# Kernel tuning notes

Hardware: AMD Instinct MI355X
Metric: run time of the kernel (lower is better)

## Reference

```python
import jax, jax.numpy as jnp
import numpy as np
from jax import lax

S, L, V, E, H, FA, HOP, NL = 512, 128, 50000, 256, 256, 128, 4, 16


def setup_inputs() -> dict:
    key = jax.random.key(0)
    ks = jax.random.split(key, 25)
    def rn(k, shape, s=0.05):
        return jax.random.normal(k, shape, dtype=jnp.float32) * s
    inp = {}
    inp['tokens'] = jax.random.randint(ks[0], (S, L), 0, V)
    inp['emb'] = rn(ks[1], (V, E), 0.1)
    # token bi-LSTM, pytorch gate layout (i,f,g,o) stacked in dim 0
    inp['tWih_f'] = rn(ks[2], (4*H, E)); inp['tWhh_f'] = rn(ks[3], (4*H, H))
    inp['tbih_f'] = rn(ks[4], (4*H,));  inp['tbhh_f'] = rn(ks[5], (4*H,))
    inp['tWih_b'] = rn(ks[6], (4*H, E)); inp['tWhh_b'] = rn(ks[7], (4*H, H))
    inp['tbih_b'] = rn(ks[8], (4*H,));  inp['tbhh_b'] = rn(ks[9], (4*H,))
    inp['attW'] = rn(ks[10], (FA, H)); inp['attb'] = rn(ks[11], (FA,))
    inp['ctx'] = rn(ks[12], (HOP, FA))
    D2 = H * HOP
    inp['sWih_f'] = rn(ks[13], (4*HOP, D2)); inp['sWhh_f'] = rn(ks[14], (4*HOP, HOP))
    inp['sbih_f'] = rn(ks[15], (4*HOP,));    inp['sbhh_f'] = rn(ks[16], (4*HOP,))
    inp['sWih_b'] = rn(ks[17], (4*HOP, D2)); inp['sWhh_b'] = rn(ks[18], (4*HOP, HOP))
    inp['sbih_b'] = rn(ks[19], (4*HOP,));    inp['sbhh_b'] = rn(ks[20], (4*HOP,))
    inp['linW'] = rn(ks[21], (NL, HOP), 0.3); inp['linb'] = rn(ks[22], (NL,), 0.3)
    inp['trans'] = rn(ks[23], (NL, NL), 1.0)
    return inp


def _lstm_dir(x, Wih, Whh, bih, bhh, reverse):
    # x: [B, T, D] -> [B, T, Hh]
    if reverse:
        x = x[:, ::-1]
    B = x.shape[0]
    Hh = Whh.shape[1]
    def step(carry, xt):
        h, c = carry
        g = xt @ Wih.T + bih + h @ Whh.T + bhh
        i, f, gg, o = jnp.split(g, 4, axis=-1)
        c = jax.nn.sigmoid(f) * c + jax.nn.sigmoid(i) * jnp.tanh(gg)
        h = jax.nn.sigmoid(o) * jnp.tanh(c)
        return (h, c), h
    h0 = jnp.zeros((B, Hh), x.dtype)
    _, hs = lax.scan(step, (h0, h0), x.transpose(1, 0, 2))
    out = hs.transpose(1, 0, 2)
    return out[:, ::-1] if reverse else out


def _bilstm_sum(x, Wf, Uf, bif, bhf, Wb, Ub, bib, bhb):
    # bidirectional LSTM; module sums fwd/bwd halves of concat output
    return (_lstm_dir(x, Wf, Uf, bif, bhf, False)
            + _lstm_dir(x, Wb, Ub, bib, bhb, True))


def _viterbi(p, T):
    # max-plus recurrence: v_n[j] = p_n[j] + max_i(v_{n-1}[i] + T[i,j])
    def step(v, pn):
        v2 = pn + jnp.max(v[:, None] + T, axis=0)
        return v2, v2
    v0 = p[0]
    _, vs = lax.scan(step, v0, p[1:])
    return jnp.concatenate([v0[None, :], vs], axis=0)  # [S, NL]


def reference(tokens, emb, tWih_f, tWhh_f, tbih_f, tbhh_f, tWih_b, tWhh_b,
              tbih_b, tbhh_b, attW, attb, ctx, sWih_f, sWhh_f, sbih_f, sbhh_f,
              sWih_b, sWhh_b, sbih_b, sbhh_b, linW, linb, trans):
    x = emb[tokens]                                   # [S, L, E] gather
    enc = _bilstm_sum(x, tWih_f, tWhh_f, tbih_f, tbhh_f,
                      tWih_b, tWhh_b, tbih_b, tbhh_b)  # [S, L, H]
    hidden = enc @ attW.T + attb                       # [S, L, FA]
    scores = hidden @ ctx.T                            # [S, L, HOP]
    attn = jax.nn.softmax(scores, axis=1)              # softmax over token axis
    sent = jnp.einsum('sld,slh->sdh', enc, attn)       # [S, H, HOP]
    sent = sent.reshape(1, sent.shape[0], -1)          # [1, S, H*HOP]
    senc = _bilstm_sum(sent, sWih_f, sWhh_f, sbih_f, sbhh_f,
                       sWib := sWih_b, sWhh_b, sbih_b, sbhh_b)  # [1, S, HOP]
    pf = senc @ linW.T + linb                          # [1, S, NL]
    return _viterbi(pf[0], trans)                      # [S, NL]
```

## Files before the change

### kernel.cpp

```cpp
#include <hip/hip_runtime.h>
#include <hip/hip_bf16.h>

typedef __attribute__((ext_vector_type(8))) short short8;
typedef __attribute__((ext_vector_type(4))) float f32x4;

__device__ __forceinline__ float b2f(unsigned short u) {
    union { unsigned int i; float f; } v; v.i = ((unsigned int)u) << 16; return v.f;
}
__device__ __forceinline__ unsigned short f2b(float f) {
    union { float f; unsigned int i; } v; v.f = f;
    return (unsigned short)((v.i + 0x7FFFu + ((v.i >> 16) & 1u)) >> 16);
}
__device__ __forceinline__ float sig_f(float x) {
    return __builtin_amdgcn_rcpf(1.f + __expf(-x));
}
__device__ __forceinline__ float tanh_f(float x) {
    return 1.f - 2.f * __builtin_amdgcn_rcpf(1.f + __expf(2.f * x));
}
__device__ __forceinline__ void gll16(const void* g, void* lds) {
    __builtin_amdgcn_global_load_lds(
        (const __attribute__((address_space(1))) unsigned int*)g,
        (__attribute__((address_space(3))) unsigned int*)lds, 16, 0, 0);
}

__global__ void k_prep(const float* __restrict__ Wih_f, const float* __restrict__ Whh_f,
                       const float* __restrict__ bih_f, const float* __restrict__ bhh_f,
                       const float* __restrict__ Wih_b, const float* __restrict__ Whh_b,
                       const float* __restrict__ bih_b, const float* __restrict__ bhh_b,
                       const float* __restrict__ attW,
                       short* __restrict__ Wfrag, float* __restrict__ biasp,
                       short* __restrict__ attWfrag)
{
    int idx = blockIdx.x * blockDim.x + threadIdx.x;
    if (idx < 2 * 1024 * 512) {
        int j = idx & 7, lane = (idx >> 3) & 63, b = idx >> 9;
        int gt = b & 3, kk = (b >> 2) & 15, ng = (b >> 6) & 15, dir = b >> 10;
        int u = lane & 15;
        int k = kk * 32 + (lane >> 4) * 8 + j;
        int row = gt * 256 + ng * 16 + u;
        const float* Wih = dir ? Wih_b : Wih_f;
        const float* Whh = dir ? Whh_b : Whh_f;
        float val = (k < 256) ? Wih[row * 256 + k] : Whh[row * 256 + (k - 256)];
        Wfrag[idx] = (short)f2b(val);
    } else if (idx < 2 * 1024 * 512 + 2048) {
        int i = idx - 2 * 1024 * 512;
        int dir = i >> 10, col = i & 1023;
        int ng = col >> 6, rem = col & 63, gt = rem >> 4, u = rem & 15;
        int row = gt * 256 + ng * 16 + u;
        biasp[i] = dir ? (bih_b[row] + bhh_b[row]) : (bih_f[row] + bhh_f[row]);
    } else if (idx < 2 * 1024 * 512 + 2048 + 32768) {
        int o = idx - (2 * 1024 * 512 + 2048);
        int j = o & 7, lane = (o >> 3) & 63, b = o >> 9;
        int kk = b & 7, nt = b >> 3;
        int fa = nt * 16 + (lane & 15);
        int k = kk * 32 + (lane >> 4) * 8 + j;
        attWfrag[o] = (short)f2b(attW[fa * 256 + k]);
    }
}

__global__ void k_prep_emb(const float* __restrict__ emb, unsigned short* __restrict__ emb16)
{
    int idx = blockIdx.x * blockDim.x + threadIdx.x;
    if (idx >= 50000 * 256 / 8) return;
    const float4* s = (const float4*)(emb + (size_t)idx * 8);
    float4 a = s[0], b = s[1];
    short8 v;
    v[0] = (short)f2b(a.x); v[1] = (short)f2b(a.y);
    v[2] = (short)f2b(a.z); v[3] = (short)f2b(a.w);
    v[4] = (short)f2b(b.x); v[5] = (short)f2b(b.y);
    v[6] = (short)f2b(b.z); v[7] = (short)f2b(b.w);
    *(short8*)(emb16 + (size_t)idx * 8) = v;
}

__global__ __launch_bounds__(256) void k_tok(const int* __restrict__ tokens,
                                             const unsigned short* __restrict__ emb16,
                                             const short* __restrict__ Wfrag,
                                             const float* __restrict__ biasp,
                                             unsigned short* __restrict__ enc_f,
                                             unsigned short* __restrict__ enc_b,
                                             float* __restrict__ c_f,
                                             float* __restrict__ c_b,
                                             int t)
{
    __shared__ __align__(16) char As[64 * 1024];
    int tid = threadIdx.x;
    int bid = blockIdx.x;
    int dir = bid >> 7;
    int ng = (bid >> 3) & 15;
    int mg = bid & 7;
    int s0 = mg * 64;
    int tcol = dir ? (127 - t) : t;
    unsigned short* enc = dir ? enc_b : enc_f;
    float* cbuf = dir ? c_b : c_f;
    bool first = (t == 0);

    int lane = tid & 63, w = tid >> 6;

    {
        int sent_l = s0 + w * 16 + (lane & 15);
        int tokv = tokens[sent_l * 128 + tcol];
        int hl = first ? 0 : (dir ? (128 - t) : (t - 1));
        #pragma unroll
        for (int i = 0; i < 16; ++i) {
            int r = w * 16 + i;
            int tok_i = __shfl(tokv, i);
            int sent_i = s0 + r;
            int chunk = lane ^ (i & 7);
            const void* srcx = emb16 + (size_t)tok_i * 256 + chunk * 8;
            const void* srch = enc + ((size_t)hl * 512 + sent_i) * 256 + (chunk - 32) * 8;
            const void* src = (chunk < 32) ? srcx : srch;
            gll16(src, As + r * 1024);
        }
    }
    __syncthreads();

    f32x4 acc0 = {0.f, 0.f, 0.f, 0.f};
    f32x4 acc1 = {0.f, 0.f, 0.f, 0.f};
    f32x4 acc2 = {0.f, 0.f, 0.f, 0.f};
    f32x4 acc3 = {0.f, 0.f, 0.f, 0.f};
    int kkmax = first ? 8 : 16;
    int row = w * 16 + (lane & 15);
    const short* wbase = Wfrag + ((size_t)((dir * 16 + ng) * 16) * 4) * 512 + lane * 8;
    #pragma unroll 4
    for (int kk = 0; kk < kkmax; ++kk) {
        int byte = (kk * 32 + (lane >> 4) * 8) * 2;
        short8 a = *(const short8*)(As + row * 1024 + (byte ^ ((row & 7) << 4)));
        const short* wp = wbase + kk * 4 * 512;
        short8 b0 = *(const short8*)(wp);
        short8 b1 = *(const short8*)(wp + 512);
        short8 b2 = *(const short8*)(wp + 1024);
        short8 b3 = *(const short8*)(wp + 1536);
        acc0 = __builtin_amdgcn_mfma_f32_16x16x32_bf16(a, b0, acc0, 0, 0, 0);
        acc1 = __builtin_amdgcn_mfma_f32_16x16x32_bf16(a, b1, acc1, 0, 0, 0);
        acc2 = __builtin_amdgcn_mfma_f32_16x16x32_bf16(a, b2, acc2, 0, 0, 0);
        acc3 = __builtin_amdgcn_mfma_f32_16x16x32_bf16(a, b3, acc3, 0, 0, 0);
    }

    int u = ng * 16 + (lane & 15);
    const float* bp = biasp + dir * 1024 + ng * 64 + (lane & 15);
    float bi = bp[0], bff = bp[16], bg = bp[32], bo = bp[48];
    int tl = dir ? (127 - t) : t;
    #pragma unroll
    for (int r = 0; r < 4; ++r) {
        int sent = s0 + w * 16 + (lane >> 4) * 4 + r;
        float gi = acc0[r] + bi;
        float gf = acc1[r] + bff;
        float gg = acc2[r] + bg;
        float go = acc3[r] + bo;
        float c_old = first ? 0.f : cbuf[sent * 256 + u];
        float cn = sig_f(gf) * c_old + sig_f(gi) * tanh_f(gg);
        float h = sig_f(go) * tanh_f(cn);
        cbuf[sent * 256 + u] = cn;
        enc[((size_t)tl * 512 + sent) * 256 + u] = f2b(h);
    }
}

__global__ __launch_bounds__(256) void k_att(const unsigned short* __restrict__ enc_f,
                                             const unsigned short* __restrict__ enc_b,
                                             const short* __restrict__ attWfrag,
                                             const float* __restrict__ attb,
                                             const float* __restrict__ ctx,
                                             const float* __restrict__ sWih_f,
                                             const float* __restrict__ sWih_b,
                                             float* __restrict__ xg)
{
    __shared__ char encs[128 * 512];
    __shared__ float hid[128][129];
    __shared__ float sc[128][5];
    __shared__ float ctxs[4][128];
    __shared__ float attbs[128];
    __shared__ float sentrow[1024];
    int s = blockIdx.x;
    int tid = threadIdx.x;
    int lane = tid & 63, w = tid >> 6;

    if (tid < 128) {
        attbs[tid] = attb[tid];
        #pragma unroll
        for (int h = 0; h < 4; ++h) ctxs[h][tid] = ctx[h * 128 + tid];
    }
    {
        int r = tid >> 1, half = tid & 1;
        const unsigned short* pf_ = enc_f + ((size_t)r * 512 + s) * 256 + half * 128;
        const unsigned short* pb_ = enc_b + ((size_t)r * 512 + s) * 256 + half * 128;
        int st = (r & 7) << 1;
        #pragma unroll
        for (int i = 0; i < 16; ++i) {
            int ii = (i + st) & 15;
            short8 vf = *(const short8*)(pf_ + ii * 8);
            short8 vb = *(const short8*)(pb_ + ii * 8);
            short8 v;
            #pragma unroll
            for (int j = 0; j < 8; ++j)
                v[j] = (short)f2b(b2f((unsigned short)vf[j]) + b2f((unsigned short)vb[j]));
            int byte = half * 256 + ii * 16;
            *(short8*)(encs + r * 512 + (byte ^ ((r & 7) << 4))) = v;
        }
    }
    __syncthreads();

    {
        f32x4 acc[2][8];
        #pragma unroll
        for (int a = 0; a < 2; ++a)
            #pragma unroll
            for (int b = 0; b < 8; ++b) acc[a][b] = (f32x4){0.f, 0.f, 0.f, 0.f};
        int r0 = w * 32 + (lane & 15);
        int r1 = r0 + 16;
        for (int kk = 0; kk < 8; ++kk) {
            int byte = (kk * 32 + (lane >> 4) * 8) * 2;
            short8 a0 = *(const short8*)(encs + r0 * 512 + (byte ^ ((r0 & 7) << 4)));
            short8 a1 = *(const short8*)(encs + r1 * 512 + (byte ^ ((r1 & 7) << 4)));
            #pragma unroll
            for (int nt = 0; nt < 8; ++nt) {
                short8 b = *(const short8*)(attWfrag + ((size_t)(nt * 8 + kk)) * 512 + lane * 8);
                acc[0][nt] = __builtin_amdgcn_mfma_f32_16x16x32_bf16(a0, b, acc[0][nt], 0, 0, 0);
                acc[1][nt] = __builtin_amdgcn_mfma_f32_16x16x32_bf16(a1, b, acc[1][nt], 0, 0, 0);
            }
        }
        #pragma unroll
        for (int mt = 0; mt < 2; ++mt)
            #pragma unroll
            for (int nt = 0; nt < 8; ++nt) {
                int fa = nt * 16 + (lane & 15);
                float ab = attbs[fa];
                #pragma unroll
                for (int r = 0; r < 4; ++r) {
                    int l = w * 32 + mt * 16 + (lane >> 4) * 4 + r;
                    hid[l][fa] = acc[mt][nt][r] + ab;
                }
            }
    }
    __syncthreads();

    {
        int l = tid >> 1;
        int hb = (tid & 1) * 2;
        float d0 = 0.f, d1 = 0.f;
        for (int k = 0; k < 128; ++k) {
            float hv = hid[l][k];
            d0 += hv * ctxs[hb][k];
            d1 += hv * ctxs[hb + 1][k];
        }
        sc[l][hb] = d0;
        sc[l][hb + 1] = d1;
    }
    __syncthreads();

    {
        float v0 = sc[lane][w];
        float v1 = sc[64 + lane][w];
        float m = fmaxf(v0, v1);
        for (int off = 32; off; off >>= 1) m = fmaxf(m, __shfl_xor(m, off));
        float e0 = __expf(v0 - m), e1 = __expf(v1 - m);
        float sm = e0 + e1;
        for (int off = 32; off; off >>= 1) sm += __shfl_xor(sm, off);
        float inv = 1.f / sm;
        sc[lane][w] = e0 * inv;
        sc[64 + lane][w] = e1 * inv;
    }
    __syncthreads();

    {
        int d = tid;
        float a0 = 0.f, a1 = 0.f, a2 = 0.f, a3 = 0.f;
        int byte = d * 2;
        for (int l = 0; l < 128; ++l) {
            float e = b2f(*(const unsigned short*)(encs + l * 512 + (byte ^ ((l & 7) << 4))));
            a0 += e * sc[l][0]; a1 += e * sc[l][1]; a2 += e * sc[l][2]; a3 += e * sc[l][3];
        }
        sentrow[d * 4 + 0] = a0; sentrow[d * 4 + 1] = a1;
        sentrow[d * 4 + 2] = a2; sentrow[d * 4 + 3] = a3;
    }
    __syncthreads();

    {
        int p = tid >> 3;
        int sub = tid & 7;
        int dirq = p >> 4, j = p & 15;
        const float* wr = (dirq ? sWih_b : sWih_f) + j * 1024 + sub * 128;
        const float* sr = sentrow + sub * 128;
        float acc = 0.f;
        #pragma unroll
        for (int k = 0; k < 128; k += 4) {
            float4 wv = *(const float4*)(wr + k);
            float4 sv = *(const float4*)(sr + k);
            acc += sv.x * wv.x + sv.y * wv.y + sv.z * wv.z + sv.w * wv.w;
        }
        acc += __shfl_xor(acc, 1);
        acc += __shfl_xor(acc, 2);
        acc += __shfl_xor(acc, 4);
        if (sub == 0)
            xg[dirq * 8192 + s * 16 + (j & 3) * 4 + (j >> 2)] = acc;
    }
}

__global__ void k_slstm(const float* __restrict__ xg,
                        const float* __restrict__ sWhh_f, const float* __restrict__ sbih_f,
                        const float* __restrict__ sbhh_f,
                        const float* __restrict__ sWhh_b, const float* __restrict__ sbih_b,
                        const float* __restrict__ sbhh_b,
                        float* __restrict__ hs)
{
    __shared__ float xs[16384];
    int tid = threadIdx.x;
    for (int i = tid; i < 4096; i += 128)
        ((float4*)xs)[i] = ((const float4*)xg)[i];
    __syncthreads();

    int dir = tid >> 6, lane = tid & 63;
    int u = lane & 3;
    const float* Whh = dir ? sWhh_b : sWhh_f;
    const float* bih = dir ? sbih_b : sbih_f;
    const float* bhh = dir ? sbhh_b : sbhh_f;
    float4 wI = *(const float4*)(Whh + (0 + u) * 4);
    float4 wF = *(const float4*)(Whh + (4 + u) * 4);
    float4 wG = *(const float4*)(Whh + (8 + u) * 4);
    float4 wO = *(const float4*)(Whh + (12 + u) * 4);
    float bI = bih[u] + bhh[u];
    float bF = bih[4 + u] + bhh[4 + u];
    float bG = bih[8 + u] + bhh[8 + u];
    float bO = bih[12 + u] + bhh[12 + u];
    const float* xd = xs + dir * 8192;
    float* hd = hs + dir * 2048;
    float h0 = 0.f, h1 = 0.f, h2 = 0.f, h3 = 0.f, c = 0.f;

    int idx0 = dir ? 511 : 0;
    float4 xv = *(const float4*)(xd + idx0 * 16 + u * 4);
    for (int tt = 0; tt < 512; ++tt) {
        int cidx = dir ? (511 - tt) : tt;
        int nidx = dir ? (510 - tt) : (tt + 1);
        nidx = nidx < 0 ? 0 : (nidx > 511 ? 511 : nidx);
        float4 xn = *(const float4*)(xd + nidx * 16 + u * 4);
        float gI = xv.x + bI + h0 * wI.x + h1 * wI.y + h2 * wI.z + h3 * wI.w;
        float gF = xv.y + bF + h0 * wF.x + h1 * wF.y + h2 * wF.z + h3 * wF.w;
        float gG = xv.z + bG + h0 * wG.x + h1 * wG.y + h2 * wG.z + h3 * wG.w;
        float gO = xv.w + bO + h0 * wO.x + h1 * wO.y + h2 * wO.z + h3 * wO.w;
        c = sig_f(gF) * c + sig_f(gI) * tanh_f(gG);
        float hu = sig_f(gO) * tanh_f(c);
        h0 = __shfl(hu, 0); h1 = __shfl(hu, 1);
        h2 = __shfl(hu, 2); h3 = __shfl(hu, 3);
        if (lane == 0) {
            float4 hv = {h0, h1, h2, h3};
            *(float4*)(hd + cidx * 4) = hv;
        }
        xv = xn;
    }
}

__global__ void k_vitpf(const float* __restrict__ hs, const float* __restrict__ linW,
                        const float* __restrict__ linb, const float* __restrict__ trans,
                        float* __restrict__ out)
{
    __shared__ float pfs[8192];
    int tid = threadIdx.x;
    for (int i = tid; i < 8192; i += 256) {
        int s = i >> 4, j = i & 15;
        float acc = linb[j];
        #pragma unroll
        for (int u = 0; u < 4; ++u)
            acc += (hs[s * 4 + u] + hs[2048 + s * 4 + u]) * linW[j * 4 + u];
        pfs[i] = acc;
    }
    __syncthreads();
    if (tid < 64) {
        int j = tid & 15;
        float T[16];
        #pragma unroll
        for (int r = 0; r < 16; ++r) T[r] = trans[((j + r) & 15) * 16 + j];
        float v = pfs[j];
        if (tid < 16) out[j] = v;
        for (int t = 1; t < 512; ++t) {
            float m = -1e30f;
            #pragma unroll
            for (int r = 0; r < 16; ++r) {
                float vv = __shfl(v, (j + r) & 15);
                m = fmaxf(m, vv + T[r]);
            }
            v = pfs[t * 16 + j] + m;
            if (tid < 16) out[t * 16 + j] = v;
        }
    }
}

extern "C" void kernel_launch(void* const* d_in, const int* in_sizes, int n_in,
                              void* d_out, int out_size, void* d_ws, size_t ws_size,
                              hipStream_t stream) {
    (void)in_sizes; (void)n_in; (void)out_size; (void)ws_size;
    const int*   tokens = (const int*)d_in[0];
    const float* emb    = (const float*)d_in[1];
    const float* tWih_f = (const float*)d_in[2];
    const float* tWhh_f = (const float*)d_in[3];
    const float* tbih_f = (const float*)d_in[4];
    const float* tbhh_f = (const float*)d_in[5];
    const float* tWih_b = (const float*)d_in[6];
    const float* tWhh_b = (const float*)d_in[7];
    const float* tbih_b = (const float*)d_in[8];
    const float* tbhh_b = (const float*)d_in[9];
    const float* attW   = (const float*)d_in[10];
    const float* attb   = (const float*)d_in[11];
    const float* ctx    = (const float*)d_in[12];
    const float* sWih_f = (const float*)d_in[13];
    const float* sWhh_f = (const float*)d_in[14];
    const float* sbih_f = (const float*)d_in[15];
    const float* sbhh_f = (const float*)d_in[16];
    const float* sWih_b = (const float*)d_in[17];
    const float* sWhh_b = (const float*)d_in[18];
    const float* sbih_b = (const float*)d_in[19];
    const float* sbhh_b = (const float*)d_in[20];
    const float* linW   = (const float*)d_in[21];
    const float* linb   = (const float*)d_in[22];
    const float* trans  = (const float*)d_in[23];

    char* ws = (char*)d_ws;
    size_t off = 0;
    auto alloc = [&](size_t bytes) -> void* {
        void* p = ws + off;
        off += (bytes + 255) & ~(size_t)255;
        return p;
    };
    short* Wfrag            = (short*)alloc((size_t)2 * 1024 * 512 * 2);
    float* biasp            = (float*)alloc(2048 * 4);
    short* attWfrag         = (short*)alloc(32768 * 2);
    unsigned short* emb16   = (unsigned short*)alloc((size_t)50000 * 256 * 2);
    unsigned short* enc_f   = (unsigned short*)alloc((size_t)128 * 512 * 256 * 2);
    unsigned short* enc_b   = (unsigned short*)alloc((size_t)128 * 512 * 256 * 2);
    float* c_f              = (float*)alloc((size_t)512 * 256 * 4);
    float* c_b              = (float*)alloc((size_t)512 * 256 * 4);
    float* xg               = (float*)alloc(16384 * 4);
    float* hs               = (float*)alloc(4096 * 4);

    int prep_total = 2 * 1024 * 512 + 2048 + 32768;
    k_prep<<<(prep_total + 255) / 256, 256, 0, stream>>>(
        tWih_f, tWhh_f, tbih_f, tbhh_f, tWih_b, tWhh_b, tbih_b, tbhh_b,
        attW, Wfrag, biasp, attWfrag);
    k_prep_emb<<<(50000 * 256 / 8 + 255) / 256, 256, 0, stream>>>(emb, emb16);

    for (int t = 0; t < 128; ++t)
        k_tok<<<256, 256, 0, stream>>>(tokens, emb16, Wfrag, biasp,
                                       enc_f, enc_b, c_f, c_b, t);

    k_att<<<512, 256, 0, stream>>>(enc_f, enc_b, attWfrag, attb, ctx,
                                   sWih_f, sWih_b, xg);
    k_slstm<<<1, 128, 0, stream>>>(xg, sWhh_f, sbih_f, sbhh_f,
                                   sWhh_b, sbih_b, sbhh_b, hs);
    k_vitpf<<<1, 256, 0, stream>>>(hs, linW, linb, trans, (float*)d_out);
}
```

Measured before the change: 1.272 ms.

## Fuse token LSTM timesteps into one persistent kernel with on-chip state

```diff
diff --git a/kernel.cpp b/kernel.cpp
--- a/kernel.cpp
+++ b/kernel.cpp
@@ -72,86 +72,108 @@
     *(short8*)(emb16 + (size_t)idx * 8) = v;
 }
 
-__global__ __launch_bounds__(256) void k_tok(const int* __restrict__ tokens,
-                                             const unsigned short* __restrict__ emb16,
-                                             const short* __restrict__ Wfrag,
-                                             const float* __restrict__ biasp,
-                                             unsigned short* __restrict__ enc_f,
-                                             unsigned short* __restrict__ enc_b,
-                                             float* __restrict__ c_f,
-                                             float* __restrict__ c_b,
-                                             int t)
-{
-    __shared__ __align__(16) char As[64 * 1024];
+__global__ __launch_bounds__(1024, 4) void k_tokf(const int* __restrict__ tokens,
+                                                  const unsigned short* __restrict__ emb16,
+                                                  const short* __restrict__ Wfrag,
+                                                  const float* __restrict__ biasp,
+                                                  unsigned short* __restrict__ enc_f,
+                                                  unsigned short* __restrict__ enc_b)
+{
+    __shared__ __align__(16) char Ax[2][16 * 512];
+    __shared__ __align__(16) char Ah[2][16 * 512];
     int tid = threadIdx.x;
+    int lane = tid & 63, w = tid >> 6;
     int bid = blockIdx.x;
-    int dir = bid >> 7;
-    int ng = (bid >> 3) & 15;
-    int mg = bid & 7;
-    int s0 = mg * 64;
-    int tcol = dir ? (127 - t) : t;
+    int dir = (bid >> 2) & 1;
+    int sg = (bid & 3) | ((bid >> 3) << 2);
+    int s0 = sg * 16;
     unsigned short* enc = dir ? enc_b : enc_f;
-    float* cbuf = dir ? c_b : c_f;
-    bool first = (t == 0);
-
-    int lane = tid & 63, w = tid >> 6;
-
-    {
-        int sent_l = s0 + w * 16 + (lane & 15);
-        int tokv = tokens[sent_l * 128 + tcol];
-        int hl = first ? 0 : (dir ? (128 - t) : (t - 1));
-        #pragma unroll
-        for (int i = 0; i < 16; ++i) {
-            int r = w * 16 + i;
-            int tok_i = __shfl(tokv, i);
-            int sent_i = s0 + r;
-            int chunk = lane ^ (i & 7);
-            const void* srcx = emb16 + (size_t)tok_i * 256 + chunk * 8;
-            const void* srch = enc + ((size_t)hl * 512 + sent_i) * 256 + (chunk - 32) * 8;
-            const void* src = (chunk < 32) ? srcx : srch;
-            gll16(src, As + r * 1024);
-        }
-    }
-    __syncthreads();
-
-    f32x4 acc0 = {0.f, 0.f, 0.f, 0.f};
-    f32x4 acc1 = {0.f, 0.f, 0.f, 0.f};
-    f32x4 acc2 = {0.f, 0.f, 0.f, 0.f};
-    f32x4 acc3 = {0.f, 0.f, 0.f, 0.f};
-    int kkmax = first ? 8 : 16;
-    int row = w * 16 + (lane & 15);
-    const short* wbase = Wfrag + ((size_t)((dir * 16 + ng) * 16) * 4) * 512 + lane * 8;
-    #pragma unroll 4
-    for (int kk = 0; kk < kkmax; ++kk) {
-        int byte = (kk * 32 + (lane >> 4) * 8) * 2;
-        short8 a = *(const short8*)(As + row * 1024 + (byte ^ ((row & 7) << 4)));
-        const short* wp = wbase + kk * 4 * 512;
-        short8 b0 = *(const short8*)(wp);
-        short8 b1 = *(const short8*)(wp + 512);
-        short8 b2 = *(const short8*)(wp + 1024);
-        short8 b3 = *(const short8*)(wp + 1536);
-        acc0 = __builtin_amdgcn_mfma_f32_16x16x32_bf16(a, b0, acc0, 0, 0, 0);
-        acc1 = __builtin_amdgcn_mfma_f32_16x16x32_bf16(a, b1, acc1, 0, 0, 0);
-        acc2 = __builtin_amdgcn_mfma_f32_16x16x32_bf16(a, b2, acc2, 0, 0, 0);
-        acc3 = __builtin_amdgcn_mfma_f32_16x16x32_bf16(a, b3, acc3, 0, 0, 0);
-    }
-
-    int u = ng * 16 + (lane & 15);
-    const float* bp = biasp + dir * 1024 + ng * 64 + (lane & 15);
+
+    const short* wbase = Wfrag + ((size_t)((dir * 16 + w) * 16) * 4) * 512 + lane * 8;
+    const float* bp = biasp + dir * 1024 + w * 64 + (lane & 15);
     float bi = bp[0], bff = bp[16], bg = bp[32], bo = bp[48];
-    int tl = dir ? (127 - t) : t;
-    #pragma unroll
-    for (int r = 0; r < 4; ++r) {
-        int sent = s0 + w * 16 + (lane >> 4) * 4 + r;
-        float gi = acc0[r] + bi;
-        float gf = acc1[r] + bff;
-        float gg = acc2[r] + bg;
-        float go = acc3[r] + bo;
-        float c_old = first ? 0.f : cbuf[sent * 256 + u];
-        float cn = sig_f(gf) * c_old + sig_f(gi) * tanh_f(gg);
-        float h = sig_f(go) * tanh_f(cn);
-        cbuf[sent * 256 + u] = cn;
-        enc[((size_t)tl * 512 + sent) * 256 + u] = f2b(h);
+
+    int arow = lane & 15;
+    int abyteoff = (lane >> 4) * 16;
+    int aswz = (arow & 7) << 4;
+
+    int srow = 2 * (w & 7) + (lane >> 5);
+    int schunk = (lane & 31) ^ (srow & 7);
+    const int* tokp = tokens + (s0 + srow) * 128;
+
+    float c0 = 0.f, c1 = 0.f, c2 = 0.f, c3 = 0.f;
+
+    if (w < 8) {
+        int tcol0 = dir ? 127 : 0;
+        int tok = tokp[tcol0];
+        gll16(emb16 + (size_t)tok * 256 + schunk * 8, (char*)Ax[0] + 2 * w * 512);
+    }
+    __syncthreads();
+
+    int u = w * 16 + (lane & 15);
+    for (int t = 0; t < 128; ++t) {
+        int cur = t & 1;
+        if (t < 127 && w < 8) {
+            int tcol = dir ? (126 - t) : (t + 1);
+            int tok = tokp[tcol];
+            gll16(emb16 + (size_t)tok * 256 + schunk * 8,
+                  (char*)Ax[cur ^ 1] + 2 * w * 512);
+        }
+        f32x4 acc0 = {0.f, 0.f, 0.f, 0.f};
+        f32x4 acc1 = {0.f, 0.f, 0.f, 0.f};
+        f32x4 acc2 = {0.f, 0.f, 0.f, 0.f};
+        f32x4 acc3 = {0.f, 0.f, 0.f, 0.f};
+        const char* axb = (const char*)Ax[cur];
+        const char* ahb = (const char*)Ah[cur];
+        #pragma unroll
+        for (int kk = 0; kk < 8; ++kk) {
+            int byte = kk * 64 + abyteoff;
+            short8 a = *(const short8*)(axb + arow * 512 + (byte ^ aswz));
+            const short* wp = wbase + (size_t)kk * 2048;
+            short8 b0 = *(const short8*)(wp);
+            short8 b1 = *(const short8*)(wp + 512);
+            short8 b2 = *(const short8*)(wp + 1024);
+            short8 b3 = *(const short8*)(wp + 1536);
+            acc0 = __builtin_amdgcn_mfma_f32_16x16x32_bf16(a, b0, acc0, 0, 0, 0);
+            acc1 = __builtin_amdgcn_mfma_f32_16x16x32_bf16(a, b1, acc1, 0, 0, 0);
+            acc2 = __builtin_amdgcn_mfma_f32_16x16x32_bf16(a, b2, acc2, 0, 0, 0);
+            acc3 = __builtin_amdgcn_mfma_f32_16x16x32_bf16(a, b3, acc3, 0, 0, 0);
+        }
+        if (t) {
+            #pragma unroll
+            for (int kk = 0; kk < 8; ++kk) {
+                int byte = kk * 64 + abyteoff;
+                short8 a = *(const short8*)(ahb + arow * 512 + (byte ^ aswz));
+                const short* wp = wbase + (size_t)(8 + kk) * 2048;
+                short8 b0 = *(const short8*)(wp);
+                short8 b1 = *(const short8*)(wp + 512);
+                short8 b2 = *(const short8*)(wp + 1024);
+                short8 b3 = *(const short8*)(wp + 1536);
+                acc0 = __builtin_amdgcn_mfma_f32_16x16x32_bf16(a, b0, acc0, 0, 0, 0);
+                acc1 = __builtin_amdgcn_mfma_f32_16x16x32_bf16(a, b1, acc1, 0, 0, 0);
+                acc2 = __builtin_amdgcn_mfma_f32_16x16x32_bf16(a, b2, acc2, 0, 0, 0);
+                acc3 = __builtin_amdgcn_mfma_f32_16x16x32_bf16(a, b3, acc3, 0, 0, 0);
+            }
+        }
+        int tl = dir ? (127 - t) : t;
+        char* ahw = (char*)Ah[cur ^ 1];
+        #pragma unroll
+        for (int r = 0; r < 4; ++r) {
+            float gi = acc0[r] + bi;
+            float gf = acc1[r] + bff;
+            float gg = acc2[r] + bg;
+            float go = acc3[r] + bo;
+            float co = (r == 0) ? c0 : (r == 1) ? c1 : (r == 2) ? c2 : c3;
+            float cn = sig_f(gf) * co + sig_f(gi) * tanh_f(gg);
+            float h = sig_f(go) * tanh_f(cn);
+            if (r == 0) c0 = cn; else if (r == 1) c1 = cn;
+            else if (r == 2) c2 = cn; else c3 = cn;
+            unsigned short hb = f2b(h);
+            int hrow = (lane >> 4) * 4 + r;
+            *(unsigned short*)(ahw + hrow * 512 + ((u * 2) ^ ((hrow & 7) << 4))) = hb;
+            enc[((size_t)tl * 512 + (s0 + hrow)) * 256 + u] = hb;
+        }
+        __syncthreads();
     }
 }
 
@@ -302,49 +324,53 @@
                         const float* __restrict__ sbhh_b,
                         float* __restrict__ hs)
 {
-    __shared__ float xs[16384];
-    int tid = threadIdx.x;
-    for (int i = tid; i < 4096; i += 128)
-        ((float4*)xs)[i] = ((const float4*)xg)[i];
-    __syncthreads();
-
-    int dir = tid >> 6, lane = tid & 63;
-    int u = lane & 3;
+    __shared__ float xs[8192];
+    int dir = blockIdx.x;
+    int lane = threadIdx.x;
+    const float* xgd = xg + dir * 8192;
+    for (int i = lane; i < 2048; i += 64)
+        ((float4*)xs)[i] = ((const float4*)xgd)[i];
+    __syncthreads();
+
     const float* Whh = dir ? sWhh_b : sWhh_f;
     const float* bih = dir ? sbih_b : sbih_f;
     const float* bhh = dir ? sbhh_b : sbhh_f;
-    float4 wI = *(const float4*)(Whh + (0 + u) * 4);
-    float4 wF = *(const float4*)(Whh + (4 + u) * 4);
-    float4 wG = *(const float4*)(Whh + (8 + u) * 4);
-    float4 wO = *(const float4*)(Whh + (12 + u) * 4);
-    float bI = bih[u] + bhh[u];
-    float bF = bih[4 + u] + bhh[4 + u];
-    float bG = bih[8 + u] + bhh[8 + u];
-    float bO = bih[12 + u] + bhh[12 + u];
-    const float* xd = xs + dir * 8192;
+    float4 W[16];
+    float B[16];
+    #pragma unroll
+    for (int j = 0; j < 16; ++j) {
+        W[j] = *(const float4*)(Whh + j * 4);
+        B[j] = bih[j] + bhh[j];
+    }
     float* hd = hs + dir * 2048;
-    float h0 = 0.f, h1 = 0.f, h2 = 0.f, h3 = 0.f, c = 0.f;
-
-    int idx0 = dir ? 511 : 0;
-    float4 xv = *(const float4*)(xd + idx0 * 16 + u * 4);
+    float h0 = 0.f, h1 = 0.f, h2 = 0.f, h3 = 0.f;
+    float cA = 0.f, cB = 0.f, cC = 0.f, cD = 0.f;
+
     for (int tt = 0; tt < 512; ++tt) {
-        int cidx = dir ? (511 - tt) : tt;
-        int nidx = dir ? (510 - tt) : (tt + 1);
-        nidx = nidx < 0 ? 0 : (nidx > 511 ? 511 : nidx);
-        float4 xn = *(const float4*)(xd + nidx * 16 + u * 4);
-        float gI = xv.x + bI + h0 * wI.x + h1 * wI.y + h2 * wI.z + h3 * wI.w;
-        float gF = xv.y + bF + h0 * wF.x + h1 * wF.y + h2 * wF.z + h3 * wF.w;
-        float gG = xv.z + bG + h0 * wG.x + h1 * wG.y + h2 * wG.z + h3 * wG.w;
-        float gO = xv.w + bO + h0 * wO.x + h1 * wO.y + h2 * wO.z + h3 * wO.w;
-        c = sig_f(gF) * c + sig_f(gI) * tanh_f(gG);
-        float hu = sig_f(gO) * tanh_f(c);
-        h0 = __shfl(hu, 0); h1 = __shfl(hu, 1);
-        h2 = __shfl(hu, 2); h3 = __shfl(hu, 3);
+        int idx = dir ? (511 - tt) : tt;
+        const float* xv = xs + idx * 16;
+        float g[16];
+        #pragma unroll
+        for (int uu = 0; uu < 4; ++uu) {
+            #pragma unroll
+            for (int gt = 0; gt < 4; ++gt) {
+                int j = gt * 4 + uu;
+                g[j] = xv[uu * 4 + gt] + B[j]
+                     + h0 * W[j].x + h1 * W[j].y + h2 * W[j].z + h3 * W[j].w;
+            }
+        }
+        float i0 = sig_f(g[0]),  i1 = sig_f(g[1]),  i2 = sig_f(g[2]),  i3 = sig_f(g[3]);
+        float f0 = sig_f(g[4]),  f1 = sig_f(g[5]),  f2 = sig_f(g[6]),  f3 = sig_f(g[7]);
+        float t0 = tanh_f(g[8]), t1 = tanh_f(g[9]), t2 = tanh_f(g[10]), t3 = tanh_f(g[11]);
+        float o0 = sig_f(g[12]), o1 = sig_f(g[13]), o2 = sig_f(g[14]), o3 = sig_f(g[15]);
+        cA = f0 * cA + i0 * t0; cB = f1 * cB + i1 * t1;
+        cC = f2 * cC + i2 * t2; cD = f3 * cD + i3 * t3;
+        h0 = o0 * tanh_f(cA); h1 = o1 * tanh_f(cB);
+        h2 = o2 * tanh_f(cC); h3 = o3 * tanh_f(cD);
         if (lane == 0) {
             float4 hv = {h0, h1, h2, h3};
-            *(float4*)(hd + cidx * 4) = hv;
-        }
-        xv = xn;
+            *(float4*)(hd + idx * 4) = hv;
+        }
     }
 }
 
@@ -425,8 +451,6 @@
     unsigned short* emb16   = (unsigned short*)alloc((size_t)50000 * 256 * 2);
     unsigned short* enc_f   = (unsigned short*)alloc((size_t)128 * 512 * 256 * 2);
     unsigned short* enc_b   = (unsigned short*)alloc((size_t)128 * 512 * 256 * 2);
-    float* c_f              = (float*)alloc((size_t)512 * 256 * 4);
-    float* c_b              = (float*)alloc((size_t)512 * 256 * 4);
     float* xg               = (float*)alloc(16384 * 4);
     float* hs               = (float*)alloc(4096 * 4);
 
@@ -436,13 +460,11 @@
         attW, Wfrag, biasp, attWfrag);
     k_prep_emb<<<(50000 * 256 / 8 + 255) / 256, 256, 0, stream>>>(emb, emb16);
 
-    for (int t = 0; t < 128; ++t)
-        k_tok<<<256, 256, 0, stream>>>(tokens, emb16, Wfrag, biasp,
-                                       enc_f, enc_b, c_f, c_b, t);
+    k_tokf<<<64, 1024, 0, stream>>>(tokens, emb16, Wfrag, biasp, enc_f, enc_b);
 
     k_att<<<512, 256, 0, stream>>>(enc_f, enc_b, attWfrag, attb, ctx,
                                    sWih_f, sWih_b, xg);
-    k_slstm<<<1, 128, 0, stream>>>(xg, sWhh_f, sbih_f, sbhh_f,
-                                   sWhh_b, sbih_b, sbhh_b, hs);
+    k_slstm<<<2, 64, 0, stream>>>(xg, sWhh_f, sbih_f, sbhh_f,
+                                  sWhh_b, sbih_b, sbhh_b, hs);
     k_vitpf<<<1, 256, 0, stream>>>(hs, linW, linb, trans, (float*)d_out);
 }
```

Result: slower. 3.499 ms (+174.9%).
